# Performance work log

Measured on AMD Instinct MI355X. Metric: run time of the kernel, lower is better.

Reference implementation:

```python
import jax, jax.numpy as jnp
import numpy as np

EMBED_DIM = 64
NUM_EMB = 8192


def _conv2d(x, w, b, stride=2, pad=1):
    # x: [B,C,H,W], w: [O,I,kh,kw] -> NCHW conv, stride 2, pad 1
    y = jax.lax.conv_general_dilated(
        x, w, window_strides=(stride, stride),
        padding=[(pad, pad), (pad, pad)],
        dimension_numbers=("NCHW", "OIHW", "NCHW"))
    return y + b[None, :, None, None]


def setup_inputs() -> dict:
    key = jax.random.key(0)
    ks = jax.random.split(key, 8)
    x = jax.random.normal(ks[0], (16, 3, 256, 256), dtype=jnp.float32)
    # Kaiming-ish small init for conv params
    w1 = jax.random.normal(ks[1], (32, 3, 4, 4), dtype=jnp.float32) * 0.1
    b1 = jnp.zeros((32,), dtype=jnp.float32)
    w2 = jax.random.normal(ks[2], (64, 32, 4, 4), dtype=jnp.float32) * 0.05
    b2 = jnp.zeros((64,), dtype=jnp.float32)
    w3 = jax.random.normal(ks[3], (EMBED_DIM, 64, 4, 4), dtype=jnp.float32) * 0.05
    b3 = jnp.zeros((EMBED_DIM,), dtype=jnp.float32)
    # codebook init uniform(-1/K, 1/K) as in torch module
    codebook = jax.random.uniform(ks[4], (NUM_EMB, EMBED_DIM), dtype=jnp.float32,
                                  minval=-1.0 / NUM_EMB, maxval=1.0 / NUM_EMB)
    return {"x": x, "w1": w1, "b1": b1, "w2": w2, "b2": b2,
            "w3": w3, "b3": b3, "codebook": codebook}


def reference(x, w1, b1, w2, b2, w3, b3, codebook):
    h = jax.nn.relu(_conv2d(x, w1, b1))
    h = jax.nn.relu(_conv2d(h, w2, b2))
    z = jax.nn.relu(_conv2d(h, w3, b3))          # [B, D, 32, 32]
    z_cl = jnp.transpose(z, (0, 2, 3, 1))        # [B, 32, 32, D]
    flat = z_cl.reshape(-1, EMBED_DIM)           # [N, D]
    dists = (jnp.sum(flat * flat, axis=1, keepdims=True)
             + jnp.sum(codebook * codebook, axis=1)
             - 2.0 * jnp.matmul(flat, codebook.T))  # [N, K]
    idx = jnp.argmin(dists, axis=1)              # [N]
    idx = idx.reshape(x.shape[0], -1)            # [B, 1024]
    return idx, jnp.float32(0.0)
```

## Files before the change

### kernel.cpp

```cpp
#include <hip/hip_runtime.h>
#include <float.h>


#define TAU 4e-6f

typedef __attribute__((ext_vector_type(8))) short s16x8;
typedef __attribute__((ext_vector_type(4))) float f32x4;
typedef unsigned short ushort_t;
typedef unsigned long long u64;

static __device__ __forceinline__ unsigned short f2bf(float f) {
    unsigned u = __float_as_uint(f);
    u = (u + 0x7fffu + ((u >> 16) & 1u)) >> 16;
    return (unsigned short)u;
}
static __device__ __forceinline__ float bf2f(unsigned short h) {
    return __uint_as_float(((unsigned)h) << 16);
}

__global__ __launch_bounds__(256) void conv1_kernel(const float* __restrict__ in,
                                                    const float* __restrict__ w,
                                                    const float* __restrict__ bias,
                                                    float* __restrict__ out) {
    int p = blockIdx.x * 256 + threadIdx.x;
    int ow = p & 127, oh = (p >> 7) & 127, bb = p >> 14;
    int oc0 = blockIdx.y * 16;
    float taps[48];
    for (int ic = 0; ic < 3; ++ic) {
        const float* ip = in + (bb * 3 + ic) * 65536;
        #pragma unroll
        for (int kh = 0; kh < 4; ++kh) {
            int ih = oh * 2 - 1 + kh;
            #pragma unroll
            for (int kw = 0; kw < 4; ++kw) {
                int iw = ow * 2 - 1 + kw;
                bool ok = ((unsigned)ih < 256u) && ((unsigned)iw < 256u);
                taps[ic * 16 + kh * 4 + kw] = ok ? ip[ih * 256 + iw] : 0.0f;
            }
        }
    }
    float* op = out + bb * (32 * 16384) + oh * 128 + ow;
    for (int oc = oc0; oc < oc0 + 16; ++oc) {
        float acc = 0.0f;
        const float* wp = w + oc * 48;
        #pragma unroll
        for (int t = 0; t < 48; ++t) acc = __fmaf_rn(taps[t], wp[t], acc);
        acc = __fadd_rn(acc, bias[oc]);
        op[oc * 16384] = fmaxf(acc, 0.0f);
    }
}

__global__ __launch_bounds__(256) void conv2_kernel(const float* __restrict__ in,
                                                    const float* __restrict__ w,
                                                    const float* __restrict__ bias,
                                                    float* __restrict__ out) {
    int p = blockIdx.x * 256 + threadIdx.x;
    int ow = p & 63, oh = (p >> 6) & 63, bb = p >> 12;
    int oc0 = blockIdx.y * 8;
    float acc[8];
    #pragma unroll
    for (int j = 0; j < 8; ++j) acc[j] = 0.0f;
    const float* ibase = in + bb * 32 * 16384;

    float r0[4], r1[4];
    #pragma unroll
    for (int kh = 0; kh < 4; ++kh) {
        int ih = oh * 2 - 1 + kh;
        float v0 = 0.0f, v1 = 0.0f;
        if ((unsigned)ih < 128u) {
            float2 t = *(const float2*)(ibase + ih * 128 + 2 * ow);
            v0 = t.x; v1 = t.y;
        }
        r0[kh] = v0; r1[kh] = v1;
    }
    for (int ic = 0; ic < 32; ++ic) {
        float n0[4], n1[4];
        int icn = (ic < 31) ? ic + 1 : 31;
        const float* ipn = ibase + icn * 16384;
        #pragma unroll
        for (int kh = 0; kh < 4; ++kh) {
            int ih = oh * 2 - 1 + kh;
            float v0 = 0.0f, v1 = 0.0f;
            if ((unsigned)ih < 128u) {
                float2 t = *(const float2*)(ipn + ih * 128 + 2 * ow);
                v0 = t.x; v1 = t.y;
            }
            n0[kh] = v0; n1[kh] = v1;
        }
        const float* wic = w + ic * 16;
        #pragma unroll
        for (int kh = 0; kh < 4; ++kh) {
            float t0 = __shfl_up(r1[kh], 1);
            if (ow == 0) t0 = 0.0f;
            float t3 = __shfl_down(r0[kh], 1);
            if (ow == 63) t3 = 0.0f;
            const float* wk = wic + kh * 4;
            #pragma unroll
            for (int j = 0; j < 8; ++j) acc[j] = __fmaf_rn(t0,     wk[(oc0 + j) * 512 + 0], acc[j]);
            #pragma unroll
            for (int j = 0; j < 8; ++j) acc[j] = __fmaf_rn(r0[kh], wk[(oc0 + j) * 512 + 1], acc[j]);
            #pragma unroll
            for (int j = 0; j < 8; ++j) acc[j] = __fmaf_rn(r1[kh], wk[(oc0 + j) * 512 + 2], acc[j]);
            #pragma unroll
            for (int j = 0; j < 8; ++j) acc[j] = __fmaf_rn(t3,     wk[(oc0 + j) * 512 + 3], acc[j]);
        }
        #pragma unroll
        for (int kh = 0; kh < 4; ++kh) { r0[kh] = n0[kh]; r1[kh] = n1[kh]; }
    }
    float* op = out + bb * (64 * 4096) + oh * 64 + ow;
    #pragma unroll
    for (int j = 0; j < 8; ++j) {
        float y = __fadd_rn(acc[j], bias[oc0 + j]);
        op[(oc0 + j) * 4096] = fmaxf(y, 0.0f);
    }
}

__global__ __launch_bounds__(256) void conv3_kernel(const float* __restrict__ in,
                                                    const float* __restrict__ w,
                                                    const float* __restrict__ bias,
                                                    float* __restrict__ flat) {
    int p = blockIdx.x * 256 + threadIdx.x;
    int ow = p & 31, oh = (p >> 5) & 31, bb = p >> 10;
    int oc0 = blockIdx.y * 4;
    float acc[4];
    #pragma unroll
    for (int j = 0; j < 4; ++j) acc[j] = 0.0f;
    const float* ibase = in + bb * 64 * 4096;

    float r0[4], r1[4];
    #pragma unroll
    for (int kh = 0; kh < 4; ++kh) {
        int ih = oh * 2 - 1 + kh;
        float v0 = 0.0f, v1 = 0.0f;
        if ((unsigned)ih < 64u) {
            float2 t = *(const float2*)(ibase + ih * 64 + 2 * ow);
            v0 = t.x; v1 = t.y;
        }
        r0[kh] = v0; r1[kh] = v1;
    }
    for (int ic = 0; ic < 64; ++ic) {
        float n0[4], n1[4];
        int icn = (ic < 63) ? ic + 1 : 63;
        const float* ipn = ibase + icn * 4096;
        #pragma unroll
        for (int kh = 0; kh < 4; ++kh) {
            int ih = oh * 2 - 1 + kh;
            float v0 = 0.0f, v1 = 0.0f;
            if ((unsigned)ih < 64u) {
                float2 t = *(const float2*)(ipn + ih * 64 + 2 * ow);
                v0 = t.x; v1 = t.y;
            }
            n0[kh] = v0; n1[kh] = v1;
        }
        const float* wic = w + ic * 16;
        #pragma unroll
        for (int kh = 0; kh < 4; ++kh) {
            float t0 = __shfl_up(r1[kh], 1);
            if (ow == 0) t0 = 0.0f;
            float t3 = __shfl_down(r0[kh], 1);
            if (ow == 31) t3 = 0.0f;
            const float* wk = wic + kh * 4;
            #pragma unroll
            for (int j = 0; j < 4; ++j) acc[j] = __fmaf_rn(t0,     wk[(oc0 + j) * 1024 + 0], acc[j]);
            #pragma unroll
            for (int j = 0; j < 4; ++j) acc[j] = __fmaf_rn(r0[kh], wk[(oc0 + j) * 1024 + 1], acc[j]);
            #pragma unroll
            for (int j = 0; j < 4; ++j) acc[j] = __fmaf_rn(r1[kh], wk[(oc0 + j) * 1024 + 2], acc[j]);
            #pragma unroll
            for (int j = 0; j < 4; ++j) acc[j] = __fmaf_rn(t3,     wk[(oc0 + j) * 1024 + 3], acc[j]);
        }
        #pragma unroll
        for (int kh = 0; kh < 4; ++kh) { r0[kh] = n0[kh]; r1[kh] = n1[kh]; }
    }
    float* op = flat + (size_t)p * 64 + oc0;
    #pragma unroll
    for (int j = 0; j < 4; ++j) {
        float y = __fadd_rn(acc[j], bias[oc0 + j]);
        op[j] = fmaxf(y, 0.0f);
    }
}

__global__ __launch_bounds__(256) void rownorm_kernel(const float* __restrict__ flat,
                                                      const float* __restrict__ cb,
                                                      float* __restrict__ sx,
                                                      float* __restrict__ sc) {
    int i = blockIdx.x * 256 + threadIdx.x;
    const float* src;
    float* dst;
    if (i < 16384) { src = flat + (size_t)i * 64; dst = sx + i; }
    else           { src = cb + (size_t)(i - 16384) * 64; dst = sc + (i - 16384); }
    float r[8];
    #pragma unroll
    for (int j = 0; j < 8; ++j) r[j] = __fmul_rn(src[j], src[j]);
    #pragma unroll
    for (int b = 1; b < 8; ++b)
        #pragma unroll
        for (int j = 0; j < 8; ++j)
            r[j] = __fadd_rn(r[j], __fmul_rn(src[b * 8 + j], src[b * 8 + j]));
    float s01 = __fadd_rn(r[0], r[1]), s23 = __fadd_rn(r[2], r[3]);
    float s45 = __fadd_rn(r[4], r[5]), s67 = __fadd_rn(r[6], r[7]);
    *dst = __fadd_rn(__fadd_rn(s01, s23), __fadd_rn(s45, s67));
}

__global__ __launch_bounds__(256) void split_kernel(const float* __restrict__ flat,
                                                    const float* __restrict__ cb,
                                                    ushort_t* __restrict__ xh,
                                                    ushort_t* __restrict__ xl,
                                                    ushort_t* __restrict__ ch,
                                                    ushort_t* __restrict__ cl,
                                                    int* __restrict__ count,
                                                    float* __restrict__ out) {
    int i = blockIdx.x * 256 + threadIdx.x;
    if (i == 0) { *count = 0; out[16384] = 0.0f; }
    float v;
    ushort_t *ph, *pl;
    if (i < 1048576) { v = flat[i]; ph = xh + i; pl = xl + i; }
    else             { int j = i - 1048576; v = cb[j]; ph = ch + j; pl = cl + j; }
    unsigned short h = f2bf(v);
    unsigned short l = f2bf(v - bf2f(h));
    *ph = h; *pl = l;
}

__global__ __launch_bounds__(512) void vq_screen_kernel(const ushort_t* __restrict__ xh,
                                                        const ushort_t* __restrict__ xl,
                                                        const ushort_t* __restrict__ ch,
                                                        const ushort_t* __restrict__ cl,
                                                        const float* __restrict__ sc,
                                                        float* __restrict__ out,
                                                        int* __restrict__ count,
                                                        int* __restrict__ list,
                                                        u64* __restrict__ qbest) {
    __shared__ float lm1[8][64];
    __shared__ int   li1[8][64];
    __shared__ float lm2[8][64];
    int tid = threadIdx.x;
    int row0 = blockIdx.x * 64;
    int w = tid >> 6, lane = tid & 63;
    int le = lane & 15, lk = lane >> 4;

    s16x8 a[4][4];
    #pragma unroll
    for (int i = 0; i < 4; ++i) {
        size_t ar = (size_t)(row0 + i * 16 + le) * 64 + lk * 8;
        a[i][0] = *(const s16x8*)(xh + ar);
        a[i][1] = *(const s16x8*)(xh + ar + 32);
        a[i][2] = *(const s16x8*)(xl + ar);
        a[i][3] = *(const s16x8*)(xl + ar + 32);
    }

    float m1[16], m2[16];
    int i1[16];
    #pragma unroll
    for (int s = 0; s < 16; ++s) { m1[s] = FLT_MAX; m2[s] = FLT_MAX; i1[s] = 0x7fffffff; }

    int colbase = w * 16 + le;
    s16x8 bh0, bh1, bl0, bl1;
    float scv;
    {
        size_t br = (size_t)colbase * 64 + lk * 8;
        bh0 = *(const s16x8*)(ch + br);
        bh1 = *(const s16x8*)(ch + br + 32);
        bl0 = *(const s16x8*)(cl + br);
        bl1 = *(const s16x8*)(cl + br + 32);
        scv = sc[colbase];
    }

    for (int nb = 0; nb < 64; ++nb) {
        int ncol = ((nb + 1) & 63) * 128 + colbase;
        size_t nbr = (size_t)ncol * 64 + lk * 8;
        s16x8 nh0 = *(const s16x8*)(ch + nbr);
        s16x8 nh1 = *(const s16x8*)(ch + nbr + 32);
        s16x8 nl0 = *(const s16x8*)(cl + nbr);
        s16x8 nl1 = *(const s16x8*)(cl + nbr + 32);
        float nsc = sc[ncol];

        f32x4 acc[4];
        #pragma unroll
        for (int i = 0; i < 4; ++i) acc[i] = (f32x4){0.f, 0.f, 0.f, 0.f};
        #pragma unroll
        for (int i = 0; i < 4; ++i) acc[i] = __builtin_amdgcn_mfma_f32_16x16x32_bf16(a[i][0], bh0, acc[i], 0, 0, 0);
        #pragma unroll
        for (int i = 0; i < 4; ++i) acc[i] = __builtin_amdgcn_mfma_f32_16x16x32_bf16(a[i][1], bh1, acc[i], 0, 0, 0);
        #pragma unroll
        for (int i = 0; i < 4; ++i) acc[i] = __builtin_amdgcn_mfma_f32_16x16x32_bf16(a[i][0], bl0, acc[i], 0, 0, 0);
        #pragma unroll
        for (int i = 0; i < 4; ++i) acc[i] = __builtin_amdgcn_mfma_f32_16x16x32_bf16(a[i][1], bl1, acc[i], 0, 0, 0);
        #pragma unroll
        for (int i = 0; i < 4; ++i) acc[i] = __builtin_amdgcn_mfma_f32_16x16x32_bf16(a[i][2], bh0, acc[i], 0, 0, 0);
        #pragma unroll
        for (int i = 0; i < 4; ++i) acc[i] = __builtin_amdgcn_mfma_f32_16x16x32_bf16(a[i][3], bh1, acc[i], 0, 0, 0);

        int col = nb * 128 + colbase;
        #pragma unroll
        for (int i = 0; i < 4; ++i) {
            #pragma unroll
            for (int reg = 0; reg < 4; ++reg) {
                int s = i * 4 + reg;
                float g = __fmaf_rn(-2.0f, acc[i][reg], scv);
                float om1 = m1[s];
                m2[s] = __builtin_amdgcn_fmed3f(om1, m2[s], g);
                i1[s] = (g < om1) ? col : i1[s];
                m1[s] = fminf(om1, g);
            }
        }
        bh0 = nh0; bh1 = nh1; bl0 = nl0; bl1 = nl1; scv = nsc;
    }

    #pragma unroll
    for (int i = 0; i < 4; ++i) {
        #pragma unroll
        for (int reg = 0; reg < 4; ++reg) {
            int s = i * 4 + reg;
            float v1 = m1[s], v2 = m2[s];
            int ix = i1[s];
            #pragma unroll
            for (int mask = 1; mask < 16; mask <<= 1) {
                float o1 = __shfl_xor(v1, mask);
                int oi = __shfl_xor(ix, mask);
                float o2 = __shfl_xor(v2, mask);
                float n2 = fminf(fminf(v2, o2), fmaxf(v1, o1));
                ix = (o1 < v1) ? oi : ((o1 == v1 && oi < ix) ? oi : ix);
                v1 = fminf(v1, o1);
                v2 = n2;
            }
            if (le == 0) {
                int rl = i * 16 + lk * 4 + reg;
                lm1[w][rl] = v1; li1[w][rl] = ix; lm2[w][rl] = v2;
            }
        }
    }
    __syncthreads();
    if (tid < 64) {
        float M1 = FLT_MAX, M2 = FLT_MAX;
        int I1 = 0x7fffffff;
        #pragma unroll
        for (int ww = 0; ww < 8; ++ww) {
            float a1 = lm1[ww][tid], a2 = lm2[ww][tid];
            int ai = li1[ww][tid];
            M2 = fminf(fminf(M2, a2), fmaxf(M1, a1));
            if (a1 < M1 || (a1 == M1 && ai < I1)) I1 = ai;
            M1 = fminf(M1, a1);
        }
        int row = row0 + tid;
        if (M2 - M1 >= TAU) {
            out[row] = (float)I1;
        } else {
            qbest[row] = 0xFFFFFFFFFFFFFFFFull;
            int pos = atomicAdd(count, 1);
            list[pos] = row;
        }
    }
}

#define FLDP 68
__global__ __launch_bounds__(256) void vq_fix_kernel(const float* __restrict__ flat,
                                                     const float* __restrict__ cb,
                                                     const float* __restrict__ sx,
                                                     const float* __restrict__ sc,
                                                     const int* __restrict__ count,
                                                     const int* __restrict__ list,
                                                     u64* __restrict__ qbest) {
    __shared__ float xs[64 * FLDP];
    __shared__ float cs[128 * FLDP];
    __shared__ float sxs[64], scs[128];
    __shared__ int rowids[64];
    int n = *count;
    int rb = blockIdx.x;
    if (rb * 64 >= n) return;
    int nrows = n - rb * 64; if (nrows > 64) nrows = 64;
    int cb0 = blockIdx.y * 128;
    int tid = threadIdx.x;

    #pragma unroll
    for (int s = 0; s < 4; ++s) {
        int idx = tid + 256 * s;
        int r = idx >> 4, c = idx & 15;
        int rr = rb * 64 + r; if (rr >= n) rr = n - 1;
        int row = list[rr];
        if (c == 0) { rowids[r] = row; sxs[r] = sx[row]; }
        *(float4*)&xs[r * FLDP + c * 4] = *(const float4*)(flat + (size_t)row * 64 + c * 4);
    }
    #pragma unroll
    for (int s = 0; s < 8; ++s) {
        int idx = tid + 256 * s;
        int r = idx >> 4, c = idx & 15;
        *(float4*)&cs[r * FLDP + c * 4] = *(const float4*)(cb + (size_t)(cb0 + r) * 64 + c * 4);
    }
    if (tid < 128) scs[tid] = sc[cb0 + tid];
    __syncthreads();

    int tr = tid >> 4, tc = tid & 15;
    float acc[4][8];
    #pragma unroll
    for (int i = 0; i < 4; ++i)
        #pragma unroll
        for (int j = 0; j < 8; ++j) acc[i][j] = 0.0f;

    for (int d = 0; d < 64; d += 4) {
        float4 ax[4], bc[8];
        #pragma unroll
        for (int i = 0; i < 4; ++i) ax[i] = *(const float4*)&xs[(tr + 16 * i) * FLDP + d];
        #pragma unroll
        for (int j = 0; j < 8; ++j) bc[j] = *(const float4*)&cs[(tc + 16 * j) * FLDP + d];
        #pragma unroll
        for (int i = 0; i < 4; ++i)
            #pragma unroll
            for (int j = 0; j < 8; ++j) {
                acc[i][j] = __fmaf_rn(ax[i].x, bc[j].x, acc[i][j]);
                acc[i][j] = __fmaf_rn(ax[i].y, bc[j].y, acc[i][j]);
                acc[i][j] = __fmaf_rn(ax[i].z, bc[j].z, acc[i][j]);
                acc[i][j] = __fmaf_rn(ax[i].w, bc[j].w, acc[i][j]);
            }
    }

    float best[4];
    int bidx[4];
    #pragma unroll
    for (int i = 0; i < 4; ++i) { best[i] = FLT_MAX; bidx[i] = 0x7fffffff; }
    #pragma unroll
    for (int j = 0; j < 8; ++j) {
        int k = cb0 + tc + 16 * j;
        float scj = scs[tc + 16 * j];
        #pragma unroll
        for (int i = 0; i < 4; ++i) {
            float t1 = __fadd_rn(sxs[tr + 16 * i], scj);
            float q = __fmaf_rn(-2.0f, acc[i][j], t1);
            if (q < best[i]) { best[i] = q; bidx[i] = k; }
        }
    }

    __syncthreads();
    float* rmin = cs;
    int* ridx = (int*)(cs + 1024);
    #pragma unroll
    for (int i = 0; i < 4; ++i) {
        rmin[(tr + 16 * i) * 16 + tc] = best[i];
        ridx[(tr + 16 * i) * 16 + tc] = bidx[i];
    }
    __syncthreads();
    if (tid < nrows) {
        float m = FLT_MAX; int mi = 0x7fffffff;
        for (int t2 = 0; t2 < 16; ++t2) {
            float v = rmin[tid * 16 + t2];
            int ix = ridx[tid * 16 + t2];
            if (v < m || (v == m && ix < mi)) { m = v; mi = ix; }
        }
        u64 key = ((u64)__float_as_uint(m) << 32) | (unsigned)mi;
        atomicMin(&qbest[rowids[tid]], key);
    }
}

__global__ __launch_bounds__(256) void vq_out_kernel(const int* __restrict__ count,
                                                     const int* __restrict__ list,
                                                     const u64* __restrict__ qbest,
                                                     float* __restrict__ out) {
    int pos = blockIdx.x * 256 + threadIdx.x;
    if (pos >= *count) return;
    int row = list[pos];
    out[row] = (float)(unsigned)(qbest[row] & 0xffffffffull);
}

extern "C" void kernel_launch(void* const* d_in, const int* in_sizes, int n_in,
                              void* d_out, int out_size, void* d_ws, size_t ws_size,
                              hipStream_t stream) {
    const float* x  = (const float*)d_in[0];
    const float* w1 = (const float*)d_in[1];
    const float* b1 = (const float*)d_in[2];
    const float* w2 = (const float*)d_in[3];
    const float* b2 = (const float*)d_in[4];
    const float* w3 = (const float*)d_in[5];
    const float* b3 = (const float*)d_in[6];
    const float* cb = (const float*)d_in[7];

    float* ws   = (float*)d_ws;
    float* out1 = ws;
    ushort_t* xh = (ushort_t*)(ws + 0);
    ushort_t* xl = (ushort_t*)(ws + 524288);
    ushort_t* ch = (ushort_t*)(ws + 1048576);
    ushort_t* cl = (ushort_t*)(ws + 1310720);
    float* out2 = ws + 8388608;
    float* flat = ws + 12582912;
    float* sx   = ws + 13631488;
    float* sc   = ws + 13647872;
    int*   count = (int*)(ws + 13656064);
    int*   list  = (int*)(ws + 13656320);
    u64*   qbest = (u64*)(ws + 13672704);
    float* out  = (float*)d_out;

    hipLaunchKernelGGL(conv1_kernel,  dim3(1024, 2), dim3(256), 0, stream, x, w1, b1, out1);
    hipLaunchKernelGGL(conv2_kernel,  dim3(256, 8), dim3(256), 0, stream, out1, w2, b2, out2);
    hipLaunchKernelGGL(conv3_kernel,  dim3(64, 16), dim3(256), 0, stream, out2, w3, b3, flat);
    hipLaunchKernelGGL(rownorm_kernel, dim3(96), dim3(256), 0, stream, flat, cb, sx, sc);
    hipLaunchKernelGGL(split_kernel,  dim3(6144), dim3(256), 0, stream, flat, cb, xh, xl, ch, cl, count, out);
    hipLaunchKernelGGL(vq_screen_kernel, dim3(256), dim3(512), 0, stream,
                       xh, xl, ch, cl, sc, out, count, list, qbest);
    hipLaunchKernelGGL(vq_fix_kernel, dim3(256, 64), dim3(256), 0, stream,
                       flat, cb, sx, sc, count, list, qbest);
    hipLaunchKernelGGL(vq_out_kernel, dim3(64), dim3(256), 0, stream, count, list, qbest, out);
}
```

Measured before the change: 303.3 us.

## Split VQ screen across codebook halves with merge kernel; register-tile conv2 rows

The VQ screening kernel now covers half the codebook per block (grid doubled along y) and writes partial best/second-best distances. A new merge kernel combines the two halves and applies the ambiguity threshold. The aim is to expose more parallelism, since the original 256 blocks underfill the GPU. Separately, conv2 now computes 4 output rows by 4 channels per thread instead of 1 row by 8 channels, to get more reuse of weight loads. This costs more registers and an extra kernel launch. On an exact tie between the two halves, the merge keeps the lower half's index, which matches the argmin tie-break.

```diff
diff --git a/kernel.cpp b/kernel.cpp
--- a/kernel.cpp
+++ b/kernel.cpp
@@ -55,63 +55,79 @@
                                                     const float* __restrict__ bias,
                                                     float* __restrict__ out) {
     int p = blockIdx.x * 256 + threadIdx.x;
-    int ow = p & 63, oh = (p >> 6) & 63, bb = p >> 12;
-    int oc0 = blockIdx.y * 8;
-    float acc[8];
-    #pragma unroll
-    for (int j = 0; j < 8; ++j) acc[j] = 0.0f;
+    int ow = p & 63;
+    int oh0 = (p >> 6) & 15;
+    int bb = p >> 10;
+    int oc0 = blockIdx.y * 4;
+    float acc[4][4];
+    #pragma unroll
+    for (int r = 0; r < 4; ++r)
+        #pragma unroll
+        for (int j = 0; j < 4; ++j) acc[r][j] = 0.0f;
     const float* ibase = in + bb * 32 * 16384;
 
-    float r0[4], r1[4];
-    #pragma unroll
-    for (int kh = 0; kh < 4; ++kh) {
-        int ih = oh * 2 - 1 + kh;
-        float v0 = 0.0f, v1 = 0.0f;
-        if ((unsigned)ih < 128u) {
-            float2 t = *(const float2*)(ibase + ih * 128 + 2 * ow);
-            v0 = t.x; v1 = t.y;
-        }
-        r0[kh] = v0; r1[kh] = v1;
-    }
+    float r0[4][4], r1[4][4];
+    #pragma unroll
+    for (int r = 0; r < 4; ++r)
+        #pragma unroll
+        for (int kh = 0; kh < 4; ++kh) {
+            int ih = (oh0 + 16 * r) * 2 - 1 + kh;
+            float v0 = 0.0f, v1 = 0.0f;
+            if ((unsigned)ih < 128u) {
+                float2 t = *(const float2*)(ibase + ih * 128 + 2 * ow);
+                v0 = t.x; v1 = t.y;
+            }
+            r0[r][kh] = v0; r1[r][kh] = v1;
+        }
+
     for (int ic = 0; ic < 32; ++ic) {
-        float n0[4], n1[4];
+        float n0[4][4], n1[4][4];
         int icn = (ic < 31) ? ic + 1 : 31;
         const float* ipn = ibase + icn * 16384;
         #pragma unroll
+        for (int r = 0; r < 4; ++r)
+            #pragma unroll
+            for (int kh = 0; kh < 4; ++kh) {
+                int ih = (oh0 + 16 * r) * 2 - 1 + kh;
+                float v0 = 0.0f, v1 = 0.0f;
+                if ((unsigned)ih < 128u) {
+                    float2 t = *(const float2*)(ipn + ih * 128 + 2 * ow);
+                    v0 = t.x; v1 = t.y;
+                }
+                n0[r][kh] = v0; n1[r][kh] = v1;
+            }
+        const float* wic = w + ic * 16;
+        #pragma unroll
         for (int kh = 0; kh < 4; ++kh) {
-            int ih = oh * 2 - 1 + kh;
-            float v0 = 0.0f, v1 = 0.0f;
-            if ((unsigned)ih < 128u) {
-                float2 t = *(const float2*)(ipn + ih * 128 + 2 * ow);
-                v0 = t.x; v1 = t.y;
-            }
-            n0[kh] = v0; n1[kh] = v1;
-        }
-        const float* wic = w + ic * 16;
-        #pragma unroll
-        for (int kh = 0; kh < 4; ++kh) {
-            float t0 = __shfl_up(r1[kh], 1);
-            if (ow == 0) t0 = 0.0f;
-            float t3 = __shfl_down(r0[kh], 1);
-            if (ow == 63) t3 = 0.0f;
-            const float* wk = wic + kh * 4;
-            #pragma unroll
-            for (int j = 0; j < 8; ++j) acc[j] = __fmaf_rn(t0,     wk[(oc0 + j) * 512 + 0], acc[j]);
-            #pragma unroll
-            for (int j = 0; j < 8; ++j) acc[j] = __fmaf_rn(r0[kh], wk[(oc0 + j) * 512 + 1], acc[j]);
-            #pragma unroll
-            for (int j = 0; j < 8; ++j) acc[j] = __fmaf_rn(r1[kh], wk[(oc0 + j) * 512 + 2], acc[j]);
-            #pragma unroll
-            for (int j = 0; j < 8; ++j) acc[j] = __fmaf_rn(t3,     wk[(oc0 + j) * 512 + 3], acc[j]);
-        }
-        #pragma unroll
-        for (int kh = 0; kh < 4; ++kh) { r0[kh] = n0[kh]; r1[kh] = n1[kh]; }
-    }
-    float* op = out + bb * (64 * 4096) + oh * 64 + ow;
-    #pragma unroll
-    for (int j = 0; j < 8; ++j) {
-        float y = __fadd_rn(acc[j], bias[oc0 + j]);
-        op[(oc0 + j) * 4096] = fmaxf(y, 0.0f);
+            #pragma unroll
+            for (int r = 0; r < 4; ++r) {
+                float t0 = __shfl_up(r1[r][kh], 1);
+                if (ow == 0) t0 = 0.0f;
+                float t3 = __shfl_down(r0[r][kh], 1);
+                if (ow == 63) t3 = 0.0f;
+                #pragma unroll
+                for (int j = 0; j < 4; ++j) {
+                    const float* wj = wic + (oc0 + j) * 512 + kh * 4;
+                    acc[r][j] = __fmaf_rn(t0,        wj[0], acc[r][j]);
+                    acc[r][j] = __fmaf_rn(r0[r][kh], wj[1], acc[r][j]);
+                    acc[r][j] = __fmaf_rn(r1[r][kh], wj[2], acc[r][j]);
+                    acc[r][j] = __fmaf_rn(t3,        wj[3], acc[r][j]);
+                }
+            }
+        }
+        #pragma unroll
+        for (int r = 0; r < 4; ++r)
+            #pragma unroll
+            for (int kh = 0; kh < 4; ++kh) { r0[r][kh] = n0[r][kh]; r1[r][kh] = n1[r][kh]; }
+    }
+    #pragma unroll
+    for (int r = 0; r < 4; ++r) {
+        float* op = out + bb * (64 * 4096) + (oh0 + 16 * r) * 64 + ow;
+        #pragma unroll
+        for (int j = 0; j < 4; ++j) {
+            float y = __fadd_rn(acc[r][j], bias[oc0 + j]);
+            op[(oc0 + j) * 4096] = fmaxf(y, 0.0f);
+        }
     }
 }
 
@@ -226,15 +242,16 @@
                                                         const ushort_t* __restrict__ ch,
                                                         const ushort_t* __restrict__ cl,
                                                         const float* __restrict__ sc,
-                                                        float* __restrict__ out,
-                                                        int* __restrict__ count,
-                                                        int* __restrict__ list,
-                                                        u64* __restrict__ qbest) {
+                                                        float* __restrict__ pm1,
+                                                        int* __restrict__ pi1,
+                                                        float* __restrict__ pm2) {
     __shared__ float lm1[8][64];
     __shared__ int   li1[8][64];
     __shared__ float lm2[8][64];
     int tid = threadIdx.x;
     int row0 = blockIdx.x * 64;
+    int half = blockIdx.y;
+    int kbase = half * 4096;
     int w = tid >> 6, lane = tid & 63;
     int le = lane & 15, lk = lane >> 4;
 
@@ -253,7 +270,7 @@
     #pragma unroll
     for (int s = 0; s < 16; ++s) { m1[s] = FLT_MAX; m2[s] = FLT_MAX; i1[s] = 0x7fffffff; }
 
-    int colbase = w * 16 + le;
+    int colbase = kbase + w * 16 + le;
     s16x8 bh0, bh1, bl0, bl1;
     float scv;
     {
@@ -265,8 +282,8 @@
         scv = sc[colbase];
     }
 
-    for (int nb = 0; nb < 64; ++nb) {
-        int ncol = ((nb + 1) & 63) * 128 + colbase;
+    for (int nb = 0; nb < 32; ++nb) {
+        int ncol = ((nb + 1) & 31) * 128 + colbase;
         size_t nbr = (size_t)ncol * 64 + lk * 8;
         s16x8 nh0 = *(const s16x8*)(ch + nbr);
         s16x8 nh1 = *(const s16x8*)(ch + nbr + 32);
@@ -341,14 +358,31 @@
             if (a1 < M1 || (a1 == M1 && ai < I1)) I1 = ai;
             M1 = fminf(M1, a1);
         }
-        int row = row0 + tid;
-        if (M2 - M1 >= TAU) {
-            out[row] = (float)I1;
-        } else {
-            qbest[row] = 0xFFFFFFFFFFFFFFFFull;
-            int pos = atomicAdd(count, 1);
-            list[pos] = row;
-        }
+        size_t o = (size_t)half * 16384 + row0 + tid;
+        pm1[o] = M1; pi1[o] = I1; pm2[o] = M2;
+    }
+}
+
+__global__ __launch_bounds__(256) void vq_merge_kernel(const float* __restrict__ pm1,
+                                                       const int* __restrict__ pi1,
+                                                       const float* __restrict__ pm2,
+                                                       float* __restrict__ out,
+                                                       int* __restrict__ count,
+                                                       int* __restrict__ list,
+                                                       u64* __restrict__ qbest) {
+    int row = blockIdx.x * 256 + threadIdx.x;
+    float a1 = pm1[row], b1 = pm1[16384 + row];
+    int ai = pi1[row], bi = pi1[16384 + row];
+    float a2 = pm2[row], b2 = pm2[16384 + row];
+    float M1 = fminf(a1, b1);
+    int I1 = (b1 < a1) ? bi : ai;
+    float M2 = fminf(fminf(a2, b2), fmaxf(a1, b1));
+    if (M2 - M1 >= TAU) {
+        out[row] = (float)I1;
+    } else {
+        qbest[row] = 0xFFFFFFFFFFFFFFFFull;
+        int pos = atomicAdd(count, 1);
+        list[pos] = row;
     }
 }
 
@@ -478,6 +512,9 @@
     ushort_t* xl = (ushort_t*)(ws + 524288);
     ushort_t* ch = (ushort_t*)(ws + 1048576);
     ushort_t* cl = (ushort_t*)(ws + 1310720);
+    float* pm1  = ws + 1572864;
+    int*   pi1  = (int*)(ws + 1605632);
+    float* pm2  = ws + 1638400;
     float* out2 = ws + 8388608;
     float* flat = ws + 12582912;
     float* sx   = ws + 13631488;
@@ -488,12 +525,14 @@
     float* out  = (float*)d_out;
 
     hipLaunchKernelGGL(conv1_kernel,  dim3(1024, 2), dim3(256), 0, stream, x, w1, b1, out1);
-    hipLaunchKernelGGL(conv2_kernel,  dim3(256, 8), dim3(256), 0, stream, out1, w2, b2, out2);
+    hipLaunchKernelGGL(conv2_kernel,  dim3(64, 16), dim3(256), 0, stream, out1, w2, b2, out2);
     hipLaunchKernelGGL(conv3_kernel,  dim3(64, 16), dim3(256), 0, stream, out2, w3, b3, flat);
     hipLaunchKernelGGL(rownorm_kernel, dim3(96), dim3(256), 0, stream, flat, cb, sx, sc);
     hipLaunchKernelGGL(split_kernel,  dim3(6144), dim3(256), 0, stream, flat, cb, xh, xl, ch, cl, count, out);
-    hipLaunchKernelGGL(vq_screen_kernel, dim3(256), dim3(512), 0, stream,
-                       xh, xl, ch, cl, sc, out, count, list, qbest);
+    hipLaunchKernelGGL(vq_screen_kernel, dim3(256, 2), dim3(512), 0, stream,
+                       xh, xl, ch, cl, sc, pm1, pi1, pm2);
+    hipLaunchKernelGGL(vq_merge_kernel, dim3(64), dim3(256), 0, stream,
+                       pm1, pi1, pm2, out, count, list, qbest);
     hipLaunchKernelGGL(vq_fix_kernel, dim3(256, 64), dim3(256), 0, stream,
                        flat, cb, sx, sc, count, list, qbest);
     hipLaunchKernelGGL(vq_out_kernel, dim3(64), dim3(256), 0, stream, count, list, qbest, out);
```

After: 319.5 us. 1.05x slower.
